# Kernel tuning notes

Measured on AMD Instinct MI355X. Metric: run time of the kernel, lower is better.

Reference implementation:

```python
import jax, jax.numpy as jnp
import numpy as np
from jax.scipy.linalg import cho_solve

N_OBS = 2_000_000
DIM = 16
EPS = 1e-6
LOG_DIM = 32  # module uses self.dim = 32 (param count) in the log-2pi term; faithful to source


def _block_diag_cov(params):
    # params: (32,) -> 8 blocks of 2x2, block = B @ B^T + eps*I, assembled block-diagonally
    B = params.reshape(8, 2, 2)
    blocks = jnp.einsum('nij,nkj->nik', B, B) + EPS * jnp.eye(2, dtype=params.dtype)
    idx = jnp.arange(8)
    M = jnp.zeros((8, 2, 8, 2), dtype=params.dtype).at[idx, :, idx, :].set(blocks)
    return M.reshape(16, 16)


def _transform_mu(mu, pose):
    # interleaved (x,y) points, rotate about centroid, translate to pose[:2]
    pts = jnp.stack([mu[0::2], mu[1::2]])  # (2, 8)
    centroid = jnp.mean(pts, axis=1, keepdims=True)
    ct, st = jnp.cos(pose[2]), jnp.sin(pose[2])
    R = jnp.stack([jnp.stack([ct, -st]), jnp.stack([st, ct])])  # (2,2)
    pts = R @ (pts - centroid) + pose[:2, None]
    return jnp.zeros(16, dtype=mu.dtype).at[0::2].set(pts[0]).at[1::2].set(pts[1])


def setup_inputs() -> dict:
    key = jax.random.key(0)
    k1, k2, k3, k4, k5 = jax.random.split(key, 5)
    obs = jax.random.normal(k1, (N_OBS, DIM), dtype=jnp.float32)
    mu_likelihood = jax.random.normal(k2, (DIM,), dtype=jnp.float32)
    # pose init ~ [uniform(15,25), uniform(15,25), uniform(-pi/16, pi/16)]
    u = jax.random.uniform(k3, (3,), dtype=jnp.float32)
    mu_prior_pose = jnp.array([15.0, 15.0, -np.pi / 16], jnp.float32) + u * jnp.array([10.0, 10.0, 2 * np.pi / 16], jnp.float32)
    # covariance params ~ uniform(cov_min=0.01, cov_max=10)
    Sigma_prior_params = jax.random.uniform(k4, (32,), dtype=jnp.float32, minval=0.01, maxval=10.0)
    Sigma_likelihood_params = jax.random.uniform(k5, (32,), dtype=jnp.float32, minval=0.01, maxval=10.0)
    return {
        'obs': obs,
        'mu_likelihood': mu_likelihood,
        'mu_prior_pose': mu_prior_pose,
        'Sigma_prior_params': Sigma_prior_params,
        'Sigma_likelihood_params': Sigma_likelihood_params,
    }


def reference(obs, mu_likelihood, mu_prior_pose, Sigma_prior_params, Sigma_likelihood_params):
    Sigma_prior = _block_diag_cov(Sigma_prior_params)
    Sigma_likelihood = _block_diag_cov(Sigma_likelihood_params)
    eye = jnp.eye(DIM, dtype=jnp.float32)

    L_prior = jnp.linalg.cholesky(Sigma_prior)
    prior_precision = cho_solve((L_prior, True), eye)
    L_like = jnp.linalg.cholesky(Sigma_likelihood)
    like_precision = cho_solve((L_like, True), eye)

    posterior_precision = prior_precision + like_precision
    L_post = jnp.linalg.cholesky(posterior_precision)
    Sigma_post = cho_solve((L_post, True), eye)

    mu_prior = _transform_mu(mu_likelihood, mu_prior_pose)
    mu_post = Sigma_post @ (cho_solve((L_prior, True), mu_prior) + cho_solve((L_like, True), mu_likelihood))

    diff = obs - mu_post  # (N, 16)
    # NOTE: faithful to source, which uses logdet of the *precision* and
    # quad form with Sigma_post = inv(posterior_precision)
    logdet = 2.0 * jnp.sum(jnp.log(jnp.diagonal(L_post)))
    quad = jnp.sum((diff @ Sigma_post) * diff, axis=1)  # (N,)
    log_terms = -0.5 * LOG_DIM * jnp.log(jnp.asarray(2.0 * jnp.pi, jnp.float32)) - 0.5 * logdet - 0.5 * quad
    return -jnp.sum(log_terms)
```

## Files before the change

kernel.cpp:

```cpp
#include <hip/hip_runtime.h>
#include <math.h>

#define EPS_COV 1e-6f
#define NBLOCKS 2048


__global__ __launch_bounds__(256) void quad_stream_kernel(
    const float4* __restrict__ obs4,
    const float*  __restrict__ mu_like,
    const float*  __restrict__ pose,
    const float*  __restrict__ sp_prior,
    const float*  __restrict__ sp_like,
    double*       __restrict__ partials,
    int n4)
{
    const int tid    = blockIdx.x * blockDim.x + threadIdx.x;
    const int stride = gridDim.x * blockDim.x;
    const int q = tid & 3;

    float cx = 0.f, cy = 0.f;
    #pragma unroll
    for (int i = 0; i < 8; ++i) { cx += mu_like[2*i]; cy += mu_like[2*i+1]; }
    cx *= 0.125f; cy *= 0.125f;
    const float ct = cosf(pose[2]), st = sinf(pose[2]);
    const float tx = pose[0], ty = pose[1];

    float m0=0.f, m1=0.f, m2=0.f, m3=0.f;
    float a0=0.f, b0=0.f, c0=0.f, a1=0.f, b1=0.f, c1=0.f;

    #pragma unroll
    for (int n = 0; n < 8; ++n) {
        float px = mu_like[2*n]   - cx;
        float py = mu_like[2*n+1] - cy;
        float mp0 = ct*px - st*py + tx;
        float mp1 = st*px + ct*py + ty;

        const float* p = sp_prior + 4*n;
        float s00 = p[0]*p[0] + p[1]*p[1] + EPS_COV;
        float s01 = p[0]*p[2] + p[1]*p[3];
        float s11 = p[2]*p[2] + p[3]*p[3] + EPS_COV;
        float det = s00*s11 - s01*s01;
        float Pp00 =  s11/det, Pp01 = -s01/det, Pp11 = s00/det;

        const float* l = sp_like + 4*n;
        float t00 = l[0]*l[0] + l[1]*l[1] + EPS_COV;
        float t01 = l[0]*l[2] + l[1]*l[3];
        float t11 = l[2]*l[2] + l[3]*l[3] + EPS_COV;
        float dl = t00*t11 - t01*t01;
        float Pl00 =  t11/dl, Pl01 = -t01/dl, Pl11 = t00/dl;

        float Q00 = Pp00 + Pl00, Q01 = Pp01 + Pl01, Q11 = Pp11 + Pl11;
        float dq = Q00*Q11 - Q01*Q01;
        float S00 = Q11/dq, S01 = -Q01/dq, S11v = Q00/dq;

        float ml0 = mu_like[2*n], ml1 = mu_like[2*n+1];
        float v0 = Pp00*mp0 + Pp01*mp1 + Pl00*ml0 + Pl01*ml1;
        float v1 = Pp01*mp0 + Pp11*mp1 + Pl01*ml0 + Pl11*ml1;
        float mpostx = S00*v0 + S01*v1;
        float mposty = S01*v0 + S11v*v1;

        if (n == 2*q)     { m0 = mpostx; m1 = mposty; a0 = S00; b0 = 2.f*S01; c0 = S11v; }
        if (n == 2*q + 1) { m2 = mpostx; m3 = mposty; a1 = S00; b1 = 2.f*S01; c1 = S11v; }
    }

    double accd = 0.0;
    #pragma unroll 4
    for (int i = tid; i < n4; i += stride) {
        float4 v = obs4[i];
        float d0 = v.x - m0, d1 = v.y - m1;
        float d2 = v.z - m2, d3 = v.w - m3;
        float pq = a0*d0*d0 + b0*d0*d1 + c0*d1*d1
                 + a1*d2*d2 + b1*d2*d3 + c1*d3*d3;
        accd += (double)pq;
    }

    #pragma unroll
    for (int off = 32; off > 0; off >>= 1)
        accd += __shfl_down(accd, off, 64);

    __shared__ double lds[4];
    const int wave = threadIdx.x >> 6;
    if ((threadIdx.x & 63) == 0) lds[wave] = accd;
    __syncthreads();
    if (threadIdx.x == 0)
        partials[blockIdx.x] = lds[0] + lds[1] + lds[2] + lds[3];
}

__global__ __launch_bounds__(256) void finalize_kernel(
    const double* __restrict__ partials,
    const float*  __restrict__ sp_prior,
    const float*  __restrict__ sp_like,
    float*        __restrict__ out,
    int nblocks, double n_obs)
{
    double s = 0.0;
    for (int i = threadIdx.x; i < nblocks; i += 256) s += partials[i];
    #pragma unroll
    for (int off = 32; off > 0; off >>= 1)
        s += __shfl_down(s, off, 64);
    __shared__ double lds[4];
    const int wave = threadIdx.x >> 6;
    if ((threadIdx.x & 63) == 0) lds[wave] = s;
    __syncthreads();

    if (threadIdx.x == 0) {
        double total = lds[0] + lds[1] + lds[2] + lds[3];
        double logdet = 0.0;
        for (int n = 0; n < 8; ++n) {
            const float* p = sp_prior + 4*n;
            double s00 = (double)p[0]*p[0] + (double)p[1]*p[1] + 1e-6;
            double s01 = (double)p[0]*p[2] + (double)p[1]*p[3];
            double s11 = (double)p[2]*p[2] + (double)p[3]*p[3] + 1e-6;
            double det = s00*s11 - s01*s01;
            double Pp00 = s11/det, Pp01 = -s01/det, Pp11 = s00/det;
            const float* l = sp_like + 4*n;
            double t00 = (double)l[0]*l[0] + (double)l[1]*l[1] + 1e-6;
            double t01 = (double)l[0]*l[2] + (double)l[1]*l[3];
            double t11 = (double)l[2]*l[2] + (double)l[3]*l[3] + 1e-6;
            double dl = t00*t11 - t01*t01;
            double Pl00 = t11/dl, Pl01 = -t01/dl, Pl11 = t00/dl;
            double Q00 = Pp00 + Pl00, Q01 = Pp01 + Pl01, Q11 = Pp11 + Pl11;
            logdet += log(Q00*Q11 - Q01*Q01);
        }
        const double LOG_2PI = 1.8378770664093454835606594728112;
        double c = n_obs * (16.0 * LOG_2PI + 0.5 * logdet);
        out[0] = (float)(c + 0.5 * total);
    }
}

extern "C" void kernel_launch(void* const* d_in, const int* in_sizes, int n_in,
                              void* d_out, int out_size, void* d_ws, size_t ws_size,
                              hipStream_t stream) {
    const float* obs      = (const float*)d_in[0];
    const float* mu_like  = (const float*)d_in[1];
    const float* pose     = (const float*)d_in[2];
    const float* sp_prior = (const float*)d_in[3];
    const float* sp_like  = (const float*)d_in[4];
    float* out = (float*)d_out;

    double* partials = (double*)d_ws;

    const int n_elems  = in_sizes[0];
    const int n4       = n_elems / 4;
    const double n_obs = (double)(n_elems / 16);

    quad_stream_kernel<<<NBLOCKS, 256, 0, stream>>>(
        (const float4*)obs, mu_like, pose, sp_prior, sp_like, partials, n4);

    finalize_kernel<<<1, 256, 0, stream>>>(partials, sp_prior, sp_like, out, NBLOCKS, n_obs);
}
```

Before: 199.9 us.

## Precompute posterior coefficients in setup kernel and batch eight loads per iteration

Moves the per-thread 2x2 posterior parameter derivation, which every thread of the streaming kernel repeated, into a single-thread setup kernel that writes 40 coefficients to the workspace. The streaming loop now issues eight float4 loads before computing, to keep more memory requests in flight, and accumulates in two float registers instead of converting every term to double. This adds one extra kernel launch and some float accumulation error per thread in exchange for a shorter prologue and more memory-level parallelism.

```diff
diff --git a/kernel.cpp b/kernel.cpp
--- a/kernel.cpp
+++ b/kernel.cpp
@@ -1,16 +1,61 @@
 #include <hip/hip_runtime.h>
 #include <math.h>
 
-#define EPS_COV 1e-6f
 #define NBLOCKS 2048
 
 
+__global__ void setup_kernel(const float* __restrict__ mu_like,
+                             const float* __restrict__ pose,
+                             const float* __restrict__ sp_prior,
+                             const float* __restrict__ sp_like,
+                             float* __restrict__ coef)
+{
+    if (blockIdx.x != 0 || threadIdx.x != 0) return;
+
+    double cx = 0.0, cy = 0.0;
+    for (int i = 0; i < 8; ++i) { cx += (double)mu_like[2*i]; cy += (double)mu_like[2*i+1]; }
+    cx *= 0.125; cy *= 0.125;
+    double th = (double)pose[2], ct = cos(th), st = sin(th);
+    double tx = (double)pose[0], ty = (double)pose[1];
+
+    for (int n = 0; n < 8; ++n) {
+        double px = (double)mu_like[2*n]   - cx;
+        double py = (double)mu_like[2*n+1] - cy;
+        double mp0 = ct*px - st*py + tx;
+        double mp1 = st*px + ct*py + ty;
+
+        const float* p = sp_prior + 4*n;
+        double s00 = (double)p[0]*p[0] + (double)p[1]*p[1] + 1e-6;
+        double s01 = (double)p[0]*p[2] + (double)p[1]*p[3];
+        double s11 = (double)p[2]*p[2] + (double)p[3]*p[3] + 1e-6;
+        double det = s00*s11 - s01*s01;
+        double Pp00 = s11/det, Pp01 = -s01/det, Pp11 = s00/det;
+
+        const float* l = sp_like + 4*n;
+        double t00 = (double)l[0]*l[0] + (double)l[1]*l[1] + 1e-6;
+        double t01 = (double)l[0]*l[2] + (double)l[1]*l[3];
+        double t11 = (double)l[2]*l[2] + (double)l[3]*l[3] + 1e-6;
+        double dl = t00*t11 - t01*t01;
+        double Pl00 = t11/dl, Pl01 = -t01/dl, Pl11 = t00/dl;
+
+        double Q00 = Pp00 + Pl00, Q01 = Pp01 + Pl01, Q11 = Pp11 + Pl11;
+        double dq = Q00*Q11 - Q01*Q01;
+        double S00 = Q11/dq, S01 = -Q01/dq, S11v = Q00/dq;
+
+        double ml0 = (double)mu_like[2*n], ml1 = (double)mu_like[2*n+1];
+        double v0 = Pp00*mp0 + Pp01*mp1 + Pl00*ml0 + Pl01*ml1;
+        double v1 = Pp01*mp0 + Pp11*mp1 + Pl01*ml0 + Pl11*ml1;
+        coef[2*n]   = (float)(S00*v0 + S01*v1);
+        coef[2*n+1] = (float)(S01*v0 + S11v*v1);
+        coef[16+n]  = (float)S00;
+        coef[24+n]  = (float)(2.0*S01);
+        coef[32+n]  = (float)S11v;
+    }
+}
+
 __global__ __launch_bounds__(256) void quad_stream_kernel(
     const float4* __restrict__ obs4,
-    const float*  __restrict__ mu_like,
-    const float*  __restrict__ pose,
-    const float*  __restrict__ sp_prior,
-    const float*  __restrict__ sp_like,
+    const float*  __restrict__ coef,
     double*       __restrict__ partials,
     int n4)
 {
@@ -18,61 +63,37 @@
     const int stride = gridDim.x * blockDim.x;
     const int q = tid & 3;
 
-    float cx = 0.f, cy = 0.f;
-    #pragma unroll
-    for (int i = 0; i < 8; ++i) { cx += mu_like[2*i]; cy += mu_like[2*i+1]; }
-    cx *= 0.125f; cy *= 0.125f;
-    const float ct = cosf(pose[2]), st = sinf(pose[2]);
-    const float tx = pose[0], ty = pose[1];
+    const float m0 = coef[4*q+0], m1 = coef[4*q+1];
+    const float m2 = coef[4*q+2], m3 = coef[4*q+3];
+    const float a0 = coef[16+2*q],   b0 = coef[24+2*q],   c0 = coef[32+2*q];
+    const float a1 = coef[16+2*q+1], b1 = coef[24+2*q+1], c1 = coef[32+2*q+1];
 
-    float m0=0.f, m1=0.f, m2=0.f, m3=0.f;
-    float a0=0.f, b0=0.f, c0=0.f, a1=0.f, b1=0.f, c1=0.f;
+    float acc0 = 0.f, acc1 = 0.f;
+    int i = tid;
 
-    #pragma unroll
-    for (int n = 0; n < 8; ++n) {
-        float px = mu_like[2*n]   - cx;
-        float py = mu_like[2*n+1] - cy;
-        float mp0 = ct*px - st*py + tx;
-        float mp1 = st*px + ct*py + ty;
-
-        const float* p = sp_prior + 4*n;
-        float s00 = p[0]*p[0] + p[1]*p[1] + EPS_COV;
-        float s01 = p[0]*p[2] + p[1]*p[3];
-        float s11 = p[2]*p[2] + p[3]*p[3] + EPS_COV;
-        float det = s00*s11 - s01*s01;
-        float Pp00 =  s11/det, Pp01 = -s01/det, Pp11 = s00/det;
-
-        const float* l = sp_like + 4*n;
-        float t00 = l[0]*l[0] + l[1]*l[1] + EPS_COV;
-        float t01 = l[0]*l[2] + l[1]*l[3];
-        float t11 = l[2]*l[2] + l[3]*l[3] + EPS_COV;
-        float dl = t00*t11 - t01*t01;
-        float Pl00 =  t11/dl, Pl01 = -t01/dl, Pl11 = t00/dl;
-
-        float Q00 = Pp00 + Pl00, Q01 = Pp01 + Pl01, Q11 = Pp11 + Pl11;
-        float dq = Q00*Q11 - Q01*Q01;
-        float S00 = Q11/dq, S01 = -Q01/dq, S11v = Q00/dq;
-
-        float ml0 = mu_like[2*n], ml1 = mu_like[2*n+1];
-        float v0 = Pp00*mp0 + Pp01*mp1 + Pl00*ml0 + Pl01*ml1;
-        float v1 = Pp01*mp0 + Pp11*mp1 + Pl01*ml0 + Pl11*ml1;
-        float mpostx = S00*v0 + S01*v1;
-        float mposty = S01*v0 + S11v*v1;
-
-        if (n == 2*q)     { m0 = mpostx; m1 = mposty; a0 = S00; b0 = 2.f*S01; c0 = S11v; }
-        if (n == 2*q + 1) { m2 = mpostx; m3 = mposty; a1 = S00; b1 = 2.f*S01; c1 = S11v; }
+    while (i + 7*stride < n4) {
+        float4 v[8];
+        #pragma unroll
+        for (int j = 0; j < 8; ++j) v[j] = obs4[i + j*stride];
+        #pragma unroll
+        for (int j = 0; j < 8; ++j) {
+            float d0 = v[j].x - m0, d1 = v[j].y - m1;
+            float d2 = v[j].z - m2, d3 = v[j].w - m3;
+            float t = a0*d0*d0 + b0*(d0*d1) + c0*d1*d1
+                    + a1*d2*d2 + b1*(d2*d3) + c1*d3*d3;
+            if (j & 1) acc1 += t; else acc0 += t;
+        }
+        i += 8*stride;
     }
-
-    double accd = 0.0;
-    #pragma unroll 4
-    for (int i = tid; i < n4; i += stride) {
+    for (; i < n4; i += stride) {
         float4 v = obs4[i];
         float d0 = v.x - m0, d1 = v.y - m1;
         float d2 = v.z - m2, d3 = v.w - m3;
-        float pq = a0*d0*d0 + b0*d0*d1 + c0*d1*d1
-                 + a1*d2*d2 + b1*d2*d3 + c1*d3*d3;
-        accd += (double)pq;
+        acc0 += a0*d0*d0 + b0*(d0*d1) + c0*d1*d1
+              + a1*d2*d2 + b1*(d2*d3) + c1*d3*d3;
     }
+
+    double accd = (double)acc0 + (double)acc1;
 
     #pragma unroll
     for (int off = 32; off > 0; off >>= 1)
@@ -138,14 +159,17 @@
     const float* sp_like  = (const float*)d_in[4];
     float* out = (float*)d_out;
 
-    double* partials = (double*)d_ws;
+    float*  coef     = (float*)d_ws;
+    double* partials = (double*)((char*)d_ws + 512);
 
     const int n_elems  = in_sizes[0];
     const int n4       = n_elems / 4;
     const double n_obs = (double)(n_elems / 16);
 
+    setup_kernel<<<1, 64, 0, stream>>>(mu_like, pose, sp_prior, sp_like, coef);
+
     quad_stream_kernel<<<NBLOCKS, 256, 0, stream>>>(
-        (const float4*)obs, mu_like, pose, sp_prior, sp_like, partials, n4);
+        (const float4*)obs, coef, partials, n4);
 
     finalize_kernel<<<1, 256, 0, stream>>>(partials, sp_prior, sp_like, out, NBLOCKS, n_obs);
 }
```

After: 204.1 us. 1.02x slower.
